# Kernel tuning notes

Hardware: AMD Instinct MI355X
Metric: run time of the kernel (lower is better)

## Reference

```python
import jax, jax.numpy as jnp
import numpy as np

B, N, D = 8, 1024, 256   # batch, nodes, input_size
H, HO = 4, 64            # nhead, hidden_size/nhead
T = 5                    # number of edge types (len(edges))
NEG = -1e9
EPS = 1e-6


def setup_inputs() -> dict:
    key = jax.random.key(0)
    ks = jax.random.split(key, 6)
    nodes_embed = jax.random.normal(ks[0], (B, N, D), dtype=jnp.float32)
    node_adj = jax.random.randint(ks[1], (B, N, N), 0, T + 1)  # values 0..T, 0 = no edge
    # per-head projection W: xavier-ish scale
    W = jax.random.normal(ks[2], (H, D, HO), dtype=jnp.float32) * (1.0 / np.sqrt(D))
    # per-edge-type scoring linear (2*HO -> 1), split into src/dst halves
    a_src = jax.random.normal(ks[3], (H, T, HO), dtype=jnp.float32) * 0.1
    a_dst = jax.random.normal(ks[4], (H, T, HO), dtype=jnp.float32) * 0.1
    bias = jnp.zeros((H, HO), dtype=jnp.float32)
    ln_gamma = jnp.ones((H, HO), dtype=jnp.float32)
    ln_beta = jnp.zeros((H, HO), dtype=jnp.float32)
    return {
        'nodes_embed': nodes_embed,
        'node_adj': node_adj,
        'W': W,
        'a_src': a_src,
        'a_dst': a_dst,
        'bias': bias,
        'ln_gamma': ln_gamma,
        'ln_beta': ln_beta,
    }


def reference(nodes_embed, node_adj, W, a_src, a_dst, bias, ln_gamma, ln_beta):
    # h: [B, H, N, HO] -- all heads projected at once
    h = jnp.einsum('bnd,hde->bhne', nodes_embed, W)
    # The torch code concatenates [h_i, h_j] and applies a (2*HO -> 1) linear per
    # edge type; that equals e_src[t, i] + e_dst[t, j] with the linear weight split
    # into src/dst halves. Avoids materializing the O(N^2 * 2*HO) concat tensor.
    e_src = jnp.einsum('bhne,hte->bhtn', h, a_src)  # [B, H, T, N]
    e_dst = jnp.einsum('bhne,hte->bhtn', h, a_dst)  # [B, H, T, N]
    n_types = a_src.shape[1]
    weight = jnp.zeros(h.shape[:2] + (h.shape[2], h.shape[2]), dtype=h.dtype)  # [B,H,N,N]
    for t in range(n_types):  # small fixed loop over edge types
        mask = (node_adj == t + 1).astype(h.dtype)[:, None]  # [B,1,N,N]
        weight = weight + mask * (e_src[:, :, t, :, None] + e_dst[:, :, t, None, :])
    weight = jax.nn.leaky_relu(weight, negative_slope=0.01)
    weight = jnp.where(node_adj[:, None] == 0, NEG, weight)
    attention = jax.nn.softmax(weight, axis=-1)  # [B,H,N,N]
    dst = jnp.einsum('bhij,bhje->bhie', attention, h) + bias[None, :, None, :]
    out = jax.nn.relu(dst) + h  # dropout is identity (p=0)
    # per-head LayerNorm over HO, eps=1e-6 (biased variance, as torch)
    mu = out.mean(axis=-1, keepdims=True)
    var = out.var(axis=-1, keepdims=True)
    out = (out - mu) / jnp.sqrt(var + EPS) * ln_gamma[None, :, None, :] + ln_beta[None, :, None, :]
    # concat heads: [B,H,N,HO] -> [B,N,H*HO]
    b, hh, n, e = out.shape
    return out.transpose(0, 2, 1, 3).reshape(b, n, hh * e)
```

## Files before the change

### kernel.cpp

```cpp
#include <hip/hip_runtime.h>
#include <hip/hip_bf16.h>

#define Bn 8
#define Nn 1024
#define Dn 256
#define Hn 4
#define HOn 64
#define Tn 5
#define WTR 80

typedef short bf16x8 __attribute__((ext_vector_type(8)));
typedef float f32x4 __attribute__((ext_vector_type(4)));

__device__ __forceinline__ float b2f(unsigned short u) {
    unsigned x = ((unsigned)u) << 16;
    float f;
    __builtin_memcpy(&f, &x, 4);
    return f;
}
__device__ __forceinline__ unsigned bfr(float f) {
    unsigned u;
    __builtin_memcpy(&u, &f, 4);
    return (u + 0x7FFFu + ((u >> 16) & 1u)) >> 16;
}
__device__ __forceinline__ unsigned short f2b(float f) { return (unsigned short)bfr(f); }

__global__ __launch_bounds__(256) void k_signal(float* __restrict__ out, int n) {
    int i = blockIdx.x * 256 + threadIdx.x;
    if (i < n) out[i] = 100.0f;
}

__global__ __launch_bounds__(256) void k_transpose_w(const float* __restrict__ W,
                                                     const float* __restrict__ a_src,
                                                     const float* __restrict__ a_dst,
                                                     unsigned short* __restrict__ WT) {
    __shared__ float tile[64][65];
    int h = blockIdx.x >> 2;
    int d0 = (blockIdx.x & 3) * 64;
    int c0 = threadIdx.x & 63;
    int r0 = threadIdx.x >> 6;
#pragma unroll
    for (int r = 0; r < 16; r++) {
        int d = r * 4 + r0;
        tile[d][c0] = W[((size_t)(h * Dn + d0 + d)) * HOn + c0];
    }
    __syncthreads();
#pragma unroll
    for (int r = 0; r < 16; r++) {
        int e = r * 4 + r0;
        WT[((size_t)(h * WTR + e)) * Dn + d0 + c0] = f2b(tile[c0][e]);
    }
    for (int t = r0; t < 2 * Tn; t += 4) {
        const float* av = (t < Tn) ? (a_src + (h * Tn + t) * HOn)
                                   : (a_dst + (h * Tn + t - Tn) * HOn);
        float s = 0.f;
#pragma unroll
        for (int e = 0; e < HOn; e++) s += tile[c0][e] * av[e];
        WT[((size_t)(h * WTR + 64 + t)) * Dn + d0 + c0] = f2b(s);
    }
    for (int rr = 74 + r0; rr < WTR; rr += 4)
        WT[((size_t)(h * WTR + rr)) * Dn + d0 + c0] = 0;
}

__global__ __launch_bounds__(256) void k_proj(const float* __restrict__ X,
                                              const unsigned short* __restrict__ WT,
                                              unsigned short* __restrict__ hT,
                                              float* __restrict__ e_src,
                                              float* __restrict__ e_dst) {
    int tid = threadIdx.x;
    int w = tid >> 6;
    int lane = tid & 63;
    int quad = lane >> 4;
    int l15 = lane & 15;
    int b = blockIdx.x >> 6;
    int i0 = (blockIdx.x & 63) * 16;
    int h = w;
    int bh = b * Hn + h;

    bf16x8 Bx[8];
    const float* xf = X + ((size_t)(b * Nn + i0 + l15)) * Dn + quad * 8;
#pragma unroll
    for (int kc = 0; kc < 8; kc++) {
        union { bf16x8 v; unsigned u[4]; } uu;
        const float4* xp = (const float4*)(xf + kc * 32);
        float4 A0 = xp[0], A1 = xp[1];
        __hip_bfloat162 h0 = __float22bfloat162_rn(make_float2(A0.x, A0.y));
        __hip_bfloat162 h1 = __float22bfloat162_rn(make_float2(A0.z, A0.w));
        __hip_bfloat162 h2 = __float22bfloat162_rn(make_float2(A1.x, A1.y));
        __hip_bfloat162 h3 = __float22bfloat162_rn(make_float2(A1.z, A1.w));
        __builtin_memcpy(&uu.u[0], &h0, 4);
        __builtin_memcpy(&uu.u[1], &h1, 4);
        __builtin_memcpy(&uu.u[2], &h2, 4);
        __builtin_memcpy(&uu.u[3], &h3, 4);
        Bx[kc] = uu.v;
    }

    f32x4 acc[5] = {{0.f, 0.f, 0.f, 0.f}, {0.f, 0.f, 0.f, 0.f}, {0.f, 0.f, 0.f, 0.f},
                    {0.f, 0.f, 0.f, 0.f}, {0.f, 0.f, 0.f, 0.f}};
    const unsigned short* wbase = WT + (size_t)h * WTR * Dn;
#pragma unroll
    for (int kc = 0; kc < 8; kc++) {
#pragma unroll
        for (int et = 0; et < 5; et++) {
            bf16x8 Aw = *(const bf16x8*)(wbase + (size_t)(et * 16 + l15) * Dn + kc * 32 + quad * 8);
            acc[et] = __builtin_amdgcn_mfma_f32_16x16x32_bf16(Aw, Bx[kc], acc[et], 0, 0, 0);
        }
    }

#pragma unroll
    for (int et = 0; et < 4; et++) {
#pragma unroll
        for (int reg = 0; reg < 4; reg++) {
            int e = et * 16 + quad * 4 + reg;
            hT[((size_t)bh * HOn + e) * Nn + i0 + l15] = f2b(acc[et][reg]);
        }
    }
#pragma unroll
    for (int reg = 0; reg < 4; reg++) {
        int t = quad * 4 + reg;
        if (t < Tn)
            e_src[((size_t)bh * Tn + t) * Nn + i0 + l15] = acc[4][reg];
        else if (t < 2 * Tn)
            e_dst[((size_t)bh * Tn + (t - Tn)) * Nn + i0 + l15] = acc[4][reg];
    }
}

__global__ __launch_bounds__(512) void k_attn(const int* __restrict__ adj,
                                              const float* __restrict__ e_src,
                                              const float* __restrict__ e_dst,
                                              const unsigned short* __restrict__ hT,
                                              const float* __restrict__ bias,
                                              const float* __restrict__ gamma,
                                              const float* __restrict__ beta,
                                              float* __restrict__ out) {
    __shared__ __align__(16) unsigned short p_lds[8][16][136];
    __shared__ float es2[4][16][8];
    __shared__ float l_lds[8][16];
    float* macc = (float*)&p_lds[4][0][0];

    int tid = threadIdx.x;
    int w = tid >> 6;
    int lane = tid & 63;
    int quad = lane >> 4;
    int l15 = lane & 15;
    int hh = w & 3;
    int half = w >> 2;
    int b = blockIdx.x >> 6;
    int i0 = (blockIdx.x & 63) * 16;
    int bh = b * Hn + hh;
    int J0 = half * 512;

    const int* adj_base = adj + ((size_t)(b * Nn + i0)) * Nn + J0;
    const float* edst = e_dst + (size_t)bh * Tn * Nn + J0;
    const unsigned short* hTb = hT + (size_t)bh * HOn * Nn;

    f32x4 acc[4] = {{0.f, 0.f, 0.f, 0.f}, {0.f, 0.f, 0.f, 0.f},
                    {0.f, 0.f, 0.f, 0.f}, {0.f, 0.f, 0.f, 0.f}};
    f32x4 accl = {0.f, 0.f, 0.f, 0.f};
    bf16x8 ONES;
    {
        short o = (short)0x3F80;
        ONES = (bf16x8){o, o, o, o, o, o, o, o};
    }

    int2 bufA[4], bufB[4];
#pragma unroll
    for (int r = 0; r < 4; r++) bufA[r] = *(const int2*)(adj_base + (size_t)r * Nn + 2 * lane);

    if (w < 4) {
        const float* esrc = e_src + (size_t)bh * Tn * Nn;
#pragma unroll
        for (int idx = lane; idx < 80; idx += 64) {
            int t = idx >> 4, row = idx & 15;
            es2[w][row][t] = esrc[t * Nn + i0 + row];
        }
    }
    __syncthreads();

#define P1ROW(ROW, AV)                                                          \
    {                                                                           \
        int a0 = (AV).x, a1 = (AV).y;                                           \
        int t0 = a0 - 1; t0 = (t0 < 0) ? 0 : t0;                                \
        int t1 = a1 - 1; t1 = (t1 < 0) ? 0 : t1;                                \
        float e0 = es2[hh][ROW][t0];                                            \
        float e1 = es2[hh][ROW][t1];                                            \
        float d0 = edc[0].x, d1 = edc[0].y;                                     \
        d0 = (t0 == 1) ? edc[1].x : d0; d1 = (t1 == 1) ? edc[1].y : d1;         \
        d0 = (t0 == 2) ? edc[2].x : d0; d1 = (t1 == 2) ? edc[2].y : d1;         \
        d0 = (t0 == 3) ? edc[3].x : d0; d1 = (t1 == 3) ? edc[3].y : d1;         \
        d0 = (t0 == 4) ? edc[4].x : d0; d1 = (t1 == 4) ? edc[4].y : d1;         \
        float x0 = e0 + d0; x0 = fmaxf(x0, 0.01f * x0);                         \
        float x1 = e1 + d1; x1 = fmaxf(x1, 0.01f * x1);                         \
        float p0 = __expf(x0); p0 = (a0 == 0) ? 0.f : p0;                       \
        float p1 = __expf(x1); p1 = (a1 == 0) ? 0.f : p1;                       \
        __hip_bfloat162 pp = __float22bfloat162_rn(make_float2(p0, p1));        \
        unsigned pu; __builtin_memcpy(&pu, &pp, 4);                             \
        *(unsigned*)(&p_lds[w][ROW][2 * lane]) = pu;                            \
    }

#pragma unroll 1
    for (int c = 0; c < 4; c++) {
        int jc = c * 128;
        float2 edc[Tn];
#pragma unroll
        for (int t = 0; t < Tn; t++) edc[t] = *(const float2*)(edst + t * Nn + jc + 2 * lane);
#pragma unroll
        for (int r = 0; r < 4; r++)
            bufB[r] = *(const int2*)(adj_base + (size_t)(4 + r) * Nn + jc + 2 * lane);
#pragma unroll
        for (int r = 0; r < 4; r++) P1ROW(r, bufA[r]);
#pragma unroll
        for (int r = 0; r < 4; r++)
            bufA[r] = *(const int2*)(adj_base + (size_t)(8 + r) * Nn + jc + 2 * lane);
#pragma unroll
        for (int r = 0; r < 4; r++) P1ROW(4 + r, bufB[r]);
#pragma unroll
        for (int r = 0; r < 4; r++)
            bufB[r] = *(const int2*)(adj_base + (size_t)(12 + r) * Nn + jc + 2 * lane);
#pragma unroll
        for (int r = 0; r < 4; r++) P1ROW(8 + r, bufA[r]);
        if (c < 3) {
#pragma unroll
            for (int r = 0; r < 4; r++)
                bufA[r] = *(const int2*)(adj_base + (size_t)r * Nn + jc + 128 + 2 * lane);
        }
#pragma unroll
        for (int r = 0; r < 4; r++) P1ROW(12 + r, bufB[r]);
#pragma unroll
        for (int k = 0; k < 4; k++) {
            bf16x8 Afr = *(const bf16x8*)(&p_lds[w][l15][k * 32 + quad * 8]);
            accl = __builtin_amdgcn_mfma_f32_16x16x32_bf16(Afr, ONES, accl, 0, 0, 0);
#pragma unroll
            for (int et = 0; et < 4; et++) {
                bf16x8 Bf = *(const bf16x8*)(hTb + (size_t)(et * 16 + l15) * Nn + J0 + jc + k * 32 + quad * 8);
                acc[et] = __builtin_amdgcn_mfma_f32_16x16x32_bf16(Afr, Bf, acc[et], 0, 0, 0);
            }
        }
    }
#undef P1ROW

    if (l15 == 0) {
#pragma unroll
        for (int reg = 0; reg < 4; reg++) l_lds[w][quad * 4 + reg] = accl[reg];
    }
    __syncthreads();
    if (w >= 4) {
#pragma unroll
        for (int et = 0; et < 4; et++)
#pragma unroll
            for (int reg = 0; reg < 4; reg++)
                macc[((hh * 16) + quad * 4 + reg) * 64 + et * 16 + l15] = acc[et][reg];
    }
    __syncthreads();
    if (w >= 4) return;

    float bv[4], gv[4], bev[4];
#pragma unroll
    for (int et = 0; et < 4; et++) {
        int e = et * 16 + l15;
        bv[et] = bias[hh * HOn + e];
        gv[et] = gamma[hh * HOn + e];
        bev[et] = beta[hh * HOn + e];
    }
#pragma unroll
    for (int reg = 0; reg < 4; reg++) {
        int r = quad * 4 + reg;
        int i = i0 + r;
        float lw = l_lds[w][r] + l_lds[w + 4][r];
        float linv = 1.f / fmaxf(lw, 1e-30f);
        float dv[4];
        float s = 0.f, ss = 0.f;
#pragma unroll
        for (int et = 0; et < 4; et++) {
            int e = et * 16 + l15;
            float v = (acc[et][reg] + macc[((hh * 16) + r) * 64 + e]) * linv + bv[et];
            v = (v > 0.f) ? v : 0.f;
            v += b2f(hTb[(size_t)e * Nn + i]);
            dv[et] = v;
            s += v;
            ss += v * v;
        }
#pragma unroll
        for (int off = 8; off; off >>= 1) {
            s += __shfl_xor(s, off);
            ss += __shfl_xor(ss, off);
        }
        float mean = s * (1.f / 64.f);
        float var = ss * (1.f / 64.f) - mean * mean;
        float rstd = rsqrtf(var + 1e-6f);
#pragma unroll
        for (int et = 0; et < 4; et++) {
            int e = et * 16 + l15;
            float o = (dv[et] - mean) * rstd * gv[et] + bev[et];
            out[((size_t)(b * Nn + i)) * (Hn * HOn) + hh * HOn + e] = o;
        }
    }
}

extern "C" void kernel_launch(void* const* d_in, const int* in_sizes, int n_in,
                              void* d_out, int out_size, void* d_ws, size_t ws_size,
                              hipStream_t stream) {
    const float* X = (const float*)d_in[0];
    const int* adj = (const int*)d_in[1];
    const float* W = (const float*)d_in[2];
    const float* a_src = (const float*)d_in[3];
    const float* a_dst = (const float*)d_in[4];
    const float* bias = (const float*)d_in[5];
    const float* gamma = (const float*)d_in[6];
    const float* beta = (const float*)d_in[7];
    float* out = (float*)d_out;

    char* ws = (char*)d_ws;
    size_t off = 0;
    unsigned short* hT = (unsigned short*)(ws + off);  off += (size_t)Bn * Hn * Nn * HOn * 2;
    unsigned short* WT = (unsigned short*)(ws + off);  off += (size_t)Hn * WTR * Dn * 2;
    float* e_src = (float*)(ws + off);                 off += (size_t)Bn * Hn * Tn * Nn * 4;
    float* e_dst = (float*)(ws + off);                 off += (size_t)Bn * Hn * Tn * Nn * 4;

    if (ws_size < off) {
        k_signal<<<(out_size + 255) / 256, 256, 0, stream>>>(out, out_size);
        return;
    }

    k_transpose_w<<<Hn * (Dn / 64), 256, 0, stream>>>(W, a_src, a_dst, WT);
    k_proj<<<Bn * (Nn / 16), 256, 0, stream>>>(X, WT, hT, e_src, e_dst);
    k_attn<<<Bn * (Nn / 16), 512, 0, stream>>>(adj, e_src, e_dst, hT, bias, gamma, beta, out);
}
```

Measured before the change: 151.3 us.

## Split attention key range across four wave groups with 1024-thread blocks

Doubles the block to 16 waves so each head's 1024 keys are split into four quarters instead of two, giving more waves in flight to hide adjacency-load latency. The P-tile staging buffer is halved to 8 rows per wave and fed to MFMA twice per chunk, with the other 8 rows taken from a shared zero row. The partial accumulators are then reduced across the four groups through LDS in extra synchronized phases. This trades more barriers and half-wasted MFMA work for higher parallelism per block.

```diff
diff --git a/kernel.cpp b/kernel.cpp
--- a/kernel.cpp
+++ b/kernel.cpp
@@ -125,18 +125,20 @@
     }
 }
 
-__global__ __launch_bounds__(512) void k_attn(const int* __restrict__ adj,
-                                              const float* __restrict__ e_src,
-                                              const float* __restrict__ e_dst,
-                                              const unsigned short* __restrict__ hT,
-                                              const float* __restrict__ bias,
-                                              const float* __restrict__ gamma,
-                                              const float* __restrict__ beta,
-                                              float* __restrict__ out) {
-    __shared__ __align__(16) unsigned short p_lds[8][16][136];
+__global__ __launch_bounds__(1024) void k_attn(const int* __restrict__ adj,
+                                               const float* __restrict__ e_src,
+                                               const float* __restrict__ e_dst,
+                                               const unsigned short* __restrict__ hT,
+                                               const float* __restrict__ bias,
+                                               const float* __restrict__ gamma,
+                                               const float* __restrict__ beta,
+                                               float* __restrict__ out) {
+    __shared__ __align__(16) unsigned short p_lds[16][8][136];
+    __shared__ __align__(16) unsigned short zrow[136];
     __shared__ float es2[4][16][8];
-    __shared__ float l_lds[8][16];
-    float* macc = (float*)&p_lds[4][0][0];
+    __shared__ float l_lds[16][16];
+    float* mac0 = (float*)&p_lds[0][0][0];
+    float* mac1 = (float*)&p_lds[8][0][0];
 
     int tid = threadIdx.x;
     int w = tid >> 6;
@@ -144,11 +146,11 @@
     int quad = lane >> 4;
     int l15 = lane & 15;
     int hh = w & 3;
-    int half = w >> 2;
+    int q = w >> 2;
     int b = blockIdx.x >> 6;
     int i0 = (blockIdx.x & 63) * 16;
     int bh = b * Hn + hh;
-    int J0 = half * 512;
+    int J0 = q * 256;
 
     const int* adj_base = adj + ((size_t)(b * Nn + i0)) * Nn + J0;
     const float* edst = e_dst + (size_t)bh * Tn * Nn + J0;
@@ -163,6 +165,11 @@
         ONES = (bf16x8){o, o, o, o, o, o, o, o};
     }
 
+    const unsigned short* abase1 = (l15 < 8) ? &p_lds[w][l15][0] : zrow;
+    const unsigned short* abase2 = (l15 >= 8) ? &p_lds[w][l15 - 8][0] : zrow;
+
+    if (tid < 68) ((unsigned*)zrow)[tid] = 0;
+
     int2 bufA[4], bufB[4];
 #pragma unroll
     for (int r = 0; r < 4; r++) bufA[r] = *(const int2*)(adj_base + (size_t)r * Nn + 2 * lane);
@@ -177,7 +184,7 @@
     }
     __syncthreads();
 
-#define P1ROW(ROW, AV)                                                          \
+#define P1ROW(ROW, PROW, AV)                                                    \
     {                                                                           \
         int a0 = (AV).x, a1 = (AV).y;                                           \
         int t0 = a0 - 1; t0 = (t0 < 0) ? 0 : t0;                                \
@@ -195,11 +202,23 @@
         float p1 = __expf(x1); p1 = (a1 == 0) ? 0.f : p1;                       \
         __hip_bfloat162 pp = __float22bfloat162_rn(make_float2(p0, p1));        \
         unsigned pu; __builtin_memcpy(&pu, &pp, 4);                             \
-        *(unsigned*)(&p_lds[w][ROW][2 * lane]) = pu;                            \
+        *(unsigned*)(&p_lds[w][PROW][2 * lane]) = pu;                           \
+    }
+
+#define MFMABATCH(AB, JC)                                                       \
+    _Pragma("unroll")                                                           \
+    for (int k = 0; k < 4; k++) {                                               \
+        bf16x8 Afr = *(const bf16x8*)((AB) + k * 32 + quad * 8);                \
+        accl = __builtin_amdgcn_mfma_f32_16x16x32_bf16(Afr, ONES, accl, 0, 0, 0); \
+        _Pragma("unroll")                                                       \
+        for (int et = 0; et < 4; et++) {                                        \
+            bf16x8 Bf = *(const bf16x8*)(hTb + (size_t)(et * 16 + l15) * Nn + J0 + (JC) + k * 32 + quad * 8); \
+            acc[et] = __builtin_amdgcn_mfma_f32_16x16x32_bf16(Afr, Bf, acc[et], 0, 0, 0); \
+        }                                                                       \
     }
 
 #pragma unroll 1
-    for (int c = 0; c < 4; c++) {
+    for (int c = 0; c < 2; c++) {
         int jc = c * 128;
         float2 edc[Tn];
 #pragma unroll
@@ -208,51 +227,64 @@
         for (int r = 0; r < 4; r++)
             bufB[r] = *(const int2*)(adj_base + (size_t)(4 + r) * Nn + jc + 2 * lane);
 #pragma unroll
-        for (int r = 0; r < 4; r++) P1ROW(r, bufA[r]);
+        for (int r = 0; r < 4; r++) P1ROW(r, r, bufA[r]);
 #pragma unroll
         for (int r = 0; r < 4; r++)
             bufA[r] = *(const int2*)(adj_base + (size_t)(8 + r) * Nn + jc + 2 * lane);
 #pragma unroll
-        for (int r = 0; r < 4; r++) P1ROW(4 + r, bufB[r]);
+        for (int r = 0; r < 4; r++) P1ROW(4 + r, 4 + r, bufB[r]);
+        MFMABATCH(abase1, jc);
 #pragma unroll
         for (int r = 0; r < 4; r++)
             bufB[r] = *(const int2*)(adj_base + (size_t)(12 + r) * Nn + jc + 2 * lane);
 #pragma unroll
-        for (int r = 0; r < 4; r++) P1ROW(8 + r, bufA[r]);
-        if (c < 3) {
+        for (int r = 0; r < 4; r++) P1ROW(8 + r, r, bufA[r]);
+        if (c < 1) {
 #pragma unroll
             for (int r = 0; r < 4; r++)
                 bufA[r] = *(const int2*)(adj_base + (size_t)r * Nn + jc + 128 + 2 * lane);
         }
 #pragma unroll
-        for (int r = 0; r < 4; r++) P1ROW(12 + r, bufB[r]);
-#pragma unroll
-        for (int k = 0; k < 4; k++) {
-            bf16x8 Afr = *(const bf16x8*)(&p_lds[w][l15][k * 32 + quad * 8]);
-            accl = __builtin_amdgcn_mfma_f32_16x16x32_bf16(Afr, ONES, accl, 0, 0, 0);
-#pragma unroll
-            for (int et = 0; et < 4; et++) {
-                bf16x8 Bf = *(const bf16x8*)(hTb + (size_t)(et * 16 + l15) * Nn + J0 + jc + k * 32 + quad * 8);
-                acc[et] = __builtin_amdgcn_mfma_f32_16x16x32_bf16(Afr, Bf, acc[et], 0, 0, 0);
+        for (int r = 0; r < 4; r++) P1ROW(12 + r, 4 + r, bufB[r]);
+        MFMABATCH(abase2, jc);
+    }
+#undef P1ROW
+#undef MFMABATCH
+
+    if (l15 == 0) {
+#pragma unroll
+        for (int reg = 0; reg < 4; reg++) l_lds[w][quad * 4 + reg] = accl[reg];
+    }
+    __syncthreads();
+
+    if (q == 1 || q == 2) {
+        float* m = (q == 1) ? mac0 : mac1;
+#pragma unroll
+        for (int et = 0; et < 4; et++)
+#pragma unroll
+            for (int reg = 0; reg < 4; reg++)
+                m[((hh * 16) + quad * 4 + reg) * 68 + et * 16 + l15] = acc[et][reg];
+    }
+    __syncthreads();
+    if (q == 0) {
+#pragma unroll
+        for (int et = 0; et < 4; et++)
+#pragma unroll
+            for (int reg = 0; reg < 4; reg++) {
+                int idx = ((hh * 16) + quad * 4 + reg) * 68 + et * 16 + l15;
+                acc[et][reg] += mac0[idx] + mac1[idx];
             }
-        }
-    }
-#undef P1ROW
-
-    if (l15 == 0) {
-#pragma unroll
-        for (int reg = 0; reg < 4; reg++) l_lds[w][quad * 4 + reg] = accl[reg];
-    }
-    __syncthreads();
-    if (w >= 4) {
+    }
+    __syncthreads();
+    if (q == 3) {
 #pragma unroll
         for (int et = 0; et < 4; et++)
 #pragma unroll
             for (int reg = 0; reg < 4; reg++)
-                macc[((hh * 16) + quad * 4 + reg) * 64 + et * 16 + l15] = acc[et][reg];
-    }
-    __syncthreads();
-    if (w >= 4) return;
+                mac0[((hh * 16) + quad * 4 + reg) * 68 + et * 16 + l15] = acc[et][reg];
+    }
+    __syncthreads();
+    if (q != 0) return;
 
     float bv[4], gv[4], bev[4];
 #pragma unroll
@@ -266,14 +298,14 @@
     for (int reg = 0; reg < 4; reg++) {
         int r = quad * 4 + reg;
         int i = i0 + r;
-        float lw = l_lds[w][r] + l_lds[w + 4][r];
+        float lw = l_lds[hh][r] + l_lds[hh + 4][r] + l_lds[hh + 8][r] + l_lds[hh + 12][r];
         float linv = 1.f / fmaxf(lw, 1e-30f);
         float dv[4];
         float s = 0.f, ss = 0.f;
 #pragma unroll
         for (int et = 0; et < 4; et++) {
             int e = et * 16 + l15;
-            float v = (acc[et][reg] + macc[((hh * 16) + r) * 64 + e]) * linv + bv[et];
+            float v = (acc[et][reg] + mac0[((hh * 16) + r) * 68 + e]) * linv + bv[et];
             v = (v > 0.f) ? v : 0.f;
             v += b2f(hTb[(size_t)e * Nn + i]);
             dv[et] = v;
@@ -324,5 +356,5 @@
 
     k_transpose_w<<<Hn * (Dn / 64), 256, 0, stream>>>(W, a_src, a_dst, WT);
     k_proj<<<Bn * (Nn / 16), 256, 0, stream>>>(X, WT, hT, e_src, e_dst);
-    k_attn<<<Bn * (Nn / 16), 512, 0, stream>>>(adj, e_src, e_dst, hT, bias, gamma, beta, out);
-}
+    k_attn<<<Bn * (Nn / 16), 1024, 0, stream>>>(adj, e_src, e_dst, hT, bias, gamma, beta, out);
+}
```

After: 194.4 us. 1.28x slower.
